# Performance work log

Hardware: AMD Instinct MI355X
Metric: run time of the kernel (lower is better)

## Reference

```python
import jax, jax.numpy as jnp
import numpy as np

D_MODEL, N_STATE, E_INNER, K_CONV, DT_RANK = 1024, 16, 2048, 4, 64
EPS = 1e-6

def _silu(x):
    return x * jax.nn.sigmoid(x)

def _rmsnorm(x, w):
    var = jnp.mean(x * x, axis=-1, keepdims=True)
    return x * jax.lax.rsqrt(var + EPS) * w

def _causal_dwconv(x, conv_w):
    # x: [B, L, E]; conv_w: [E, 1, K] depthwise kernel
    xc = jnp.swapaxes(x, 1, 2)  # [B, E, L]
    xc = jnp.pad(xc, ((0, 0), (0, 0), (K_CONV - 1, 0)))
    y = jax.lax.conv_general_dilated(
        xc, conv_w, window_strides=(1,), padding='VALID',
        dimension_numbers=('NCL', 'OIL', 'NCL'), feature_group_count=E_INNER)
    return jnp.swapaxes(y, 1, 2)  # [B, L, E]

def _selective_scan(u, delta, A, Bm, Cm, Dp):
    # u, delta: [B, L, E]; Bm, Cm: [B, L, N]; A: [E, N]; Dp: [E]
    def step(h, inp):
        d_t, B_t, C_t, u_t = inp  # [B,E], [B,N], [B,N], [B,E]
        dA = jnp.exp(d_t[..., None] * A)                       # [B,E,N]
        h = dA * h + (d_t * u_t)[..., None] * B_t[:, None, :]  # [B,E,N]
        y = jnp.einsum('ben,bn->be', h, C_t)
        return h, y
    h0 = jnp.zeros((u.shape[0], E_INNER, N_STATE), u.dtype)
    xs = (jnp.swapaxes(delta, 0, 1), jnp.swapaxes(Bm, 0, 1),
          jnp.swapaxes(Cm, 0, 1), jnp.swapaxes(u, 0, 1))
    h_last, ys = jax.lax.scan(step, h0, xs)
    return jnp.swapaxes(ys, 0, 1) + u * Dp, h_last

def setup_inputs() -> dict:
    key = jax.random.key(0)
    ks = jax.random.split(key, 8)
    B, L = 4, 1024
    hidden_states = jax.random.normal(ks[0], (B, L, D_MODEL), jnp.float32)
    norm_w = jnp.ones((D_MODEL,), jnp.float32)
    W_in = jax.random.normal(ks[1], (D_MODEL, 2 * E_INNER), jnp.float32) * (D_MODEL ** -0.5)
    conv_w = jax.random.normal(ks[2], (E_INNER, 1, K_CONV), jnp.float32) * (K_CONV ** -0.5)
    W_x = jax.random.normal(ks[3], (E_INNER, DT_RANK + 2 * N_STATE), jnp.float32) * (E_INNER ** -0.5)
    W_dt = jax.random.normal(ks[4], (DT_RANK, E_INNER), jnp.float32) * (DT_RANK ** -0.5)
    # dt bias so softplus(b) lands roughly in [delta_min, delta_max]
    dt = jnp.exp(jax.random.uniform(ks[5], (E_INNER,)) * (np.log(0.1) - np.log(0.001)) + np.log(0.001))
    b_dt = dt + jnp.log(-jnp.expm1(-dt))  # inverse softplus
    A_log = jnp.log(jnp.broadcast_to(jnp.arange(1, N_STATE + 1, dtype=jnp.float32), (E_INNER, N_STATE)))
    D_param = jnp.ones((E_INNER,), jnp.float32)
    W_out = jax.random.normal(ks[6], (E_INNER, D_MODEL), jnp.float32) * (E_INNER ** -0.5)
    return {"hidden_states": hidden_states, "norm_w": norm_w, "W_in": W_in,
            "conv_w": conv_w, "W_x": W_x, "W_dt": W_dt, "b_dt": b_dt,
            "A_log": A_log, "D_param": D_param, "W_out": W_out}

def reference(hidden_states, norm_w, W_in, conv_w, W_x, W_dt, b_dt, A_log, D_param, W_out):
    residual = hidden_states
    x = _rmsnorm(hidden_states, norm_w)
    xz = jnp.einsum('bld,de->ble', x, W_in)          # [B,L,2E]
    x_in, z = jnp.split(xz, 2, axis=-1)
    x_act = _silu(_causal_dwconv(x_in, conv_w))      # [B,L,E]
    x_db = jnp.einsum('ble,er->blr', x_act, W_x)     # [B,L,R+2N]
    dt_lr = x_db[..., :DT_RANK]
    Bm = x_db[..., DT_RANK:DT_RANK + N_STATE]
    Cm = x_db[..., DT_RANK + N_STATE:]
    delta = jax.nn.softplus(jnp.einsum('blr,re->ble', dt_lr, W_dt) + b_dt)
    A = -jnp.exp(A_log)
    y, h_last = _selective_scan(x_act, delta, A, Bm, Cm, D_param)
    y = y * _silu(z)
    out = jnp.einsum('ble,ed->bld', y, W_out)
    # dropout is identity in eval mode
    return residual + out, h_last
```

## Files before the change

### kernel.cpp

```cpp
#include <hip/hip_runtime.h>
#include <cstdint>
#include <cstddef>

#define DM 1024
#define EI 2048
#define NS 16
#define DR 64
#define BB 4
#define LL 1024
#define MM (BB*LL)
#define NCHUNK 32
#define CHUNK 32

typedef __attribute__((ext_vector_type(8))) __bf16 bf16x8;
typedef __attribute__((ext_vector_type(4))) float f32x4;
typedef __attribute__((ext_vector_type(8))) unsigned short u16x8;

__device__ __forceinline__ unsigned short f2bf(float f) {
    union { float f; unsigned int u; } v; v.f = f;
    unsigned int r = v.u + 0x7FFFu + ((v.u >> 16) & 1u);
    return (unsigned short)(r >> 16);
}
__device__ __forceinline__ float bf2f(unsigned short u) {
    union { unsigned int u; float f; } v; v.u = ((unsigned int)u) << 16;
    return v.f;
}

__device__ __forceinline__ void gload_lds16(const unsigned short* g, unsigned short* l) {
    __builtin_amdgcn_global_load_lds(
        (const __attribute__((address_space(1))) unsigned int*)g,
        (__attribute__((address_space(3))) unsigned int*)l, 16, 0, 0);
}

__global__ void rmsnorm_bf16(const float* __restrict__ x, const float* __restrict__ w,
                             unsigned short* __restrict__ out) {
    int m = blockIdx.x, tid = threadIdx.x;
    const float4* row = (const float4*)(x + (size_t)m * DM);
    float4 v = row[tid];
    float ss = v.x*v.x + v.y*v.y + v.z*v.z + v.w*v.w;
    #pragma unroll
    for (int o = 32; o; o >>= 1) ss += __shfl_down(ss, o);
    __shared__ float red[4];
    if ((tid & 63) == 0) red[tid >> 6] = ss;
    __syncthreads();
    ss = red[0] + red[1] + red[2] + red[3];
    float scale = rsqrtf(ss * (1.0f / DM) + 1e-6f);
    const float4* wr = (const float4*)w;
    float4 wv = wr[tid];
    ushort4 o4;
    o4.x = f2bf(v.x * scale * wv.x);
    o4.y = f2bf(v.y * scale * wv.y);
    o4.z = f2bf(v.z * scale * wv.z);
    o4.w = f2bf(v.w * scale * wv.w);
    ((ushort4*)out)[(size_t)m * (DM/4) + tid] = o4;
}

__global__ void transpose_all(const float* __restrict__ W_in, const float* __restrict__ W_x,
                              const float* __restrict__ W_dt, const float* __restrict__ W_out,
                              unsigned short* __restrict__ wt_in, unsigned short* __restrict__ wt_x,
                              unsigned short* __restrict__ wt_dt, unsigned short* __restrict__ wt_out) {
    __shared__ float t[32][33];
    int id = blockIdx.x;
    const float* in; unsigned short* out;
    int R, C, Cpad, bx, by;
    if (id < 4096)      { in = W_in;  out = wt_in;  R = 1024; C = 4096; Cpad = 4096; bx = id & 127; by = id >> 7; }
    else if (id < 4352) { id -= 4096; in = W_x;  out = wt_x;  R = 2048; C = 96;  Cpad = 128;  bx = id & 3;  by = id >> 2; }
    else if (id < 4480) { id -= 4352; in = W_dt; out = wt_dt; R = 64;   C = 2048; Cpad = 2048; bx = id & 63; by = id >> 6; }
    else                { id -= 4480; in = W_out; out = wt_out; R = 2048; C = 1024; Cpad = 1024; bx = id & 31; by = id >> 5; }
    int c0 = bx * 32, r0 = by * 32;
    int tx = threadIdx.x, ty = threadIdx.y;
    #pragma unroll
    for (int j = 0; j < 32; j += 8) {
        int r = r0 + ty + j, c = c0 + tx;
        t[ty + j][tx] = (r < R && c < C) ? in[(size_t)r * C + c] : 0.f;
    }
    __syncthreads();
    #pragma unroll
    for (int j = 0; j < 32; j += 8) {
        int c = c0 + ty + j, r = r0 + tx;
        if (c < Cpad && r < R) out[(size_t)c * R + r] = f2bf(t[tx][ty + j]);
    }
}

template<int EPI>
__global__ void gemm_mfma(const unsigned short* __restrict__ A,
                          const unsigned short* __restrict__ Bt,
                          float* __restrict__ C,
                          const float* __restrict__ ex1,
                          unsigned short* __restrict__ exb,
                          int M, int N, int K, int ldc) {
    __shared__ __attribute__((aligned(16))) unsigned short lds_a[128 * 32];
    __shared__ __attribute__((aligned(16))) unsigned short lds_b[128 * 32];
    const int tid = threadIdx.x;
    const int w = tid >> 6, lane = tid & 63;
    const int m0 = blockIdx.y * 128;
    const int n0 = (EPI == 3) ? 0 : blockIdx.x * 128;
    const int kstart = (EPI == 3) ? blockIdx.x * (K >> 3) : 0;
    const int kend   = (EPI == 3) ? kstart + (K >> 3) : K;
    const int wm = (w & 1) * 64, wn = (w >> 1) * 64;
    const int q = lane >> 4, r = lane & 15;
    const int srow = lane >> 2;
    const int scol = (lane & 3) * 8;

    f32x4 acc[4][4];
    f32x4 zero = {0.f, 0.f, 0.f, 0.f};
    #pragma unroll
    for (int i = 0; i < 4; ++i)
        #pragma unroll
        for (int j = 0; j < 4; ++j) acc[i][j] = zero;

    for (int kb = kstart; kb < kend; kb += 32) {
        __syncthreads();
        #pragma unroll
        for (int j = 0; j < 2; ++j) {
            int rbase = w * 32 + j * 16;
            gload_lds16(A  + (size_t)(m0 + rbase + srow) * K + kb + scol, lds_a + rbase * 32);
            gload_lds16(Bt + (size_t)(n0 + rbase + srow) * K + kb + scol, lds_b + rbase * 32);
        }
        __syncthreads();
        bf16x8 af[4], bfr[4];
        #pragma unroll
        for (int mi = 0; mi < 4; ++mi)
            af[mi] = *(const bf16x8*)(lds_a + (wm + mi * 16 + r) * 32 + q * 8);
        #pragma unroll
        for (int ni = 0; ni < 4; ++ni)
            bfr[ni] = *(const bf16x8*)(lds_b + (wn + ni * 16 + r) * 32 + q * 8);
        #pragma unroll
        for (int mi = 0; mi < 4; ++mi)
            #pragma unroll
            for (int ni = 0; ni < 4; ++ni)
                acc[mi][ni] = __builtin_amdgcn_mfma_f32_16x16x32_bf16(af[mi], bfr[ni], acc[mi][ni], 0, 0, 0);
    }

    #pragma unroll
    for (int mi = 0; mi < 4; ++mi) {
        #pragma unroll
        for (int ni = 0; ni < 4; ++ni) {
            f32x4 v = acc[mi][ni];
            int gmb = m0 + wm + mi * 16 + q * 4;
            int gn  = n0 + wn + ni * 16 + r;
            #pragma unroll
            for (int t = 0; t < 4; ++t) {
                int gm = gmb + t;
                float val = v[t];
                if (EPI == 1) {
                    C[(size_t)gm * ldc + gn] = val + ex1[(size_t)gm * ldc + gn];
                } else if (EPI == 2) {
                    val += ex1[gn];
                    val = fmaxf(val, 0.f) + log1pf(__expf(-fabsf(val)));
                    exb[(size_t)gm * ldc + gn] = f2bf(val);
                } else if (EPI == 3) {
                    C[((size_t)blockIdx.x * M + gm) * 128 + gn] = val;
                } else {
                    exb[(size_t)gm * ldc + gn] = f2bf(val);
                }
            }
        }
    }
}

__global__ void xproj_reduce(const float* __restrict__ Pp,
                             unsigned short* __restrict__ dtlr, float* __restrict__ bc) {
    int id = blockIdx.x * 256 + threadIdx.x;
    int n = id & 127, m = id >> 7;
    if (n >= DR + 2 * NS) return;
    float s = 0.f;
    #pragma unroll
    for (int ks = 0; ks < 8; ++ks)
        s += Pp[((size_t)ks * MM + m) * 128 + n];
    if (n < DR) dtlr[(size_t)m * DR + n] = f2bf(s);
    else bc[(size_t)m * 32 + (n - DR)] = s;
}

__global__ void conv_silu8(const unsigned short* __restrict__ xzb, const float* __restrict__ cw,
                           unsigned short* __restrict__ xab) {
    size_t idx8 = ((size_t)blockIdx.x * 256 + threadIdx.x) * 8;
    int e = (int)(idx8 & (EI - 1));
    size_t m = idx8 >> 11;
    int l = (int)(m & (LL - 1));
    u16x8 x0 = *(const u16x8*)(xzb + m * 4096 + e);
    u16x8 zer = {0,0,0,0,0,0,0,0};
    u16x8 x1 = (l >= 1) ? *(const u16x8*)(xzb + (m - 1) * 4096 + e) : zer;
    u16x8 x2 = (l >= 2) ? *(const u16x8*)(xzb + (m - 2) * 4096 + e) : zer;
    u16x8 x3 = (l >= 3) ? *(const u16x8*)(xzb + (m - 3) * 4096 + e) : zer;
    u16x8 o;
    #pragma unroll
    for (int j = 0; j < 8; ++j) {
        float4 wv = ((const float4*)cw)[e + j];
        float s = bf2f(x0[j]) * wv.w + bf2f(x1[j]) * wv.z
                + bf2f(x2[j]) * wv.y + bf2f(x3[j]) * wv.x;
        float a = s / (1.f + __expf(-s));
        o[j] = f2bf(a);
    }
    *(u16x8*)(xab + idx8) = o;
}

__global__ void scan_phase1(const unsigned short* __restrict__ dbufb, const unsigned short* __restrict__ xu,
                            const float* __restrict__ bc, const float* __restrict__ A_log,
                            float* __restrict__ P, float* __restrict__ H) {
    int e = blockIdx.x * 256 + threadIdx.x;
    int c = blockIdx.y, b = blockIdx.z;
    float A[NS], h[NS], p[NS];
    #pragma unroll
    for (int n = 0; n < NS; ++n) {
        A[n] = -expf(A_log[(size_t)e * NS + n]);
        h[n] = 0.f; p[n] = 1.f;
    }
    int mbase = b * LL + c * CHUNK;
    for (int t = 0; t < CHUNK; ++t) {
        size_t m = (size_t)(mbase + t);
        float d = bf2f(dbufb[m * 2048 + e]);
        float u = bf2f(xu[m * 2048 + e]);
        float du = d * u;
        const float* Bv = bc + m * 32;
        #pragma unroll
        for (int n = 0; n < NS; ++n) {
            float dA = __expf(d * A[n]);
            p[n] *= dA;
            h[n] = fmaf(dA, h[n], du * Bv[n]);
        }
    }
    size_t base = ((size_t)(b * NCHUNK + c) * NS) * 2048 + e;
    #pragma unroll
    for (int n = 0; n < NS; ++n) {
        P[base + (size_t)n * 2048] = p[n];
        H[base + (size_t)n * 2048] = h[n];
    }
}

__global__ void scan_phase2(const float* __restrict__ P, const float* __restrict__ H,
                            float* __restrict__ h0, float* __restrict__ hlast) {
    int id = blockIdx.x * 256 + threadIdx.x;
    int e = id & (EI - 1);
    int bn = id >> 11;
    int n = bn & (NS - 1), b = bn >> 4;
    float h = 0.f;
    #pragma unroll
    for (int c = 0; c < NCHUNK; ++c) {
        size_t ix = (((size_t)(b * NCHUNK + c) * NS) + n) * 2048 + e;
        h0[ix] = h;
        h = fmaf(P[ix], h, H[ix]);
    }
    hlast[(((size_t)b * EI + e) * NS) + n] = h;
}

__global__ void scan_phase3(const unsigned short* __restrict__ dbufb, const unsigned short* __restrict__ xu,
                            const unsigned short* __restrict__ xzb,
                            const float* __restrict__ bc, const float* __restrict__ A_log,
                            const float* __restrict__ Dp, const float* __restrict__ h0,
                            unsigned short* __restrict__ ybf) {
    int e = blockIdx.x * 256 + threadIdx.x;
    int c = blockIdx.y, b = blockIdx.z;
    float A[NS], h[NS];
    size_t base = ((size_t)(b * NCHUNK + c) * NS) * 2048 + e;
    #pragma unroll
    for (int n = 0; n < NS; ++n) {
        A[n] = -expf(A_log[(size_t)e * NS + n]);
        h[n] = h0[base + (size_t)n * 2048];
    }
    float D = Dp[e];
    int mbase = b * LL + c * CHUNK;
    for (int t = 0; t < CHUNK; ++t) {
        size_t m = (size_t)(mbase + t);
        float d = bf2f(dbufb[m * 2048 + e]);
        float u = bf2f(xu[m * 2048 + e]);
        float du = d * u;
        const float* Bv = bc + m * 32;
        float y = 0.f;
        #pragma unroll
        for (int n = 0; n < NS; ++n) {
            float dA = __expf(d * A[n]);
            h[n] = fmaf(dA, h[n], du * Bv[n]);
            y = fmaf(h[n], Bv[16 + n], y);
        }
        y = fmaf(u, D, y);
        float z = bf2f(xzb[m * 4096 + 2048 + e]);
        float sil = z / (1.f + __expf(-z));
        ybf[m * 2048 + e] = f2bf(y * sil);
    }
}

extern "C" void kernel_launch(void* const* d_in, const int* in_sizes, int n_in,
                              void* d_out, int out_size, void* d_ws, size_t ws_size,
                              hipStream_t stream) {
    (void)in_sizes; (void)n_in; (void)out_size; (void)ws_size;
    const float* hidden = (const float*)d_in[0];
    const float* norm_w = (const float*)d_in[1];
    const float* W_in   = (const float*)d_in[2];
    const float* conv_w = (const float*)d_in[3];
    const float* W_x    = (const float*)d_in[4];
    const float* W_dt   = (const float*)d_in[5];
    const float* b_dt   = (const float*)d_in[6];
    const float* A_log  = (const float*)d_in[7];
    const float* D_par  = (const float*)d_in[8];
    const float* W_out  = (const float*)d_in[9];
    float* out = (float*)d_out;
    char* ws = (char*)d_ws;
    const size_t MB = 1ull << 20;

    unsigned short* xzb      = (unsigned short*)(ws + 0);
    unsigned short* xact_bf  = (unsigned short*)(ws + 32 * MB);
    unsigned short* xnorm_bf = (unsigned short*)(ws + 48 * MB);
    unsigned short* wt_in    = (unsigned short*)(ws + 56 * MB);
    unsigned short* wt_out   = (unsigned short*)(ws + 64 * MB);
    unsigned short* wt_x     = (unsigned short*)(ws + 68 * MB);
    unsigned short* wt_dt    = (unsigned short*)(ws + 68 * MB + 512 * 1024);
    unsigned short* dtlr     = (unsigned short*)(ws + 69 * MB);
    float*          bc       = (float*)(ws + 69 * MB + 512 * 1024);
    unsigned short* dbufb    = (unsigned short*)(ws + 70 * MB);
    unsigned short* ybf      = (unsigned short*)(ws + 86 * MB);
    float*          h0       = (float*)(ws + 102 * MB);
    float*          P        = (float*)(ws + 118 * MB);
    float*          Hb       = (float*)(ws + 134 * MB);
    float* Ppart = P;
    float* hlast = out + (size_t)MM * DM;

    rmsnorm_bf16<<<MM, 256, 0, stream>>>(hidden, norm_w, xnorm_bf);
    transpose_all<<<6528, dim3(32, 8), 0, stream>>>(W_in, W_x, W_dt, W_out,
                                                    wt_in, wt_x, wt_dt, wt_out);

    gemm_mfma<4><<<dim3(32, 32), 256, 0, stream>>>(xnorm_bf, wt_in, nullptr, nullptr, xzb,
                                                   MM, 4096, 1024, 4096);
    conv_silu8<<<(MM * EI) / (256 * 8), 256, 0, stream>>>(xzb, conv_w, xact_bf);
    gemm_mfma<3><<<dim3(8, 32), 256, 0, stream>>>(xact_bf, wt_x, Ppart, nullptr, nullptr,
                                                  MM, 128, 2048, 128);
    xproj_reduce<<<(MM * 128) / 256, 256, 0, stream>>>(Ppart, dtlr, bc);
    gemm_mfma<2><<<dim3(16, 32), 256, 0, stream>>>(dtlr, wt_dt, nullptr, b_dt, dbufb,
                                                   MM, 2048, 64, 2048);
    scan_phase1<<<dim3(8, NCHUNK, BB), 256, 0, stream>>>(dbufb, xact_bf, bc, A_log, P, Hb);
    scan_phase2<<<(BB * NS * EI) / 256, 256, 0, stream>>>(P, Hb, h0, hlast);
    scan_phase3<<<dim3(8, NCHUNK, BB), 256, 0, stream>>>(dbufb, xact_bf, xzb, bc, A_log, D_par, h0, ybf);
    gemm_mfma<1><<<dim3(8, 32), 256, 0, stream>>>(ybf, wt_out, out, hidden, nullptr,
                                                  MM, 1024, 2048, 1024);
}
```

Baseline: 329.3 us.

## Replace in_proj GEMM with 256x256-tile 8-wave pipelined MFMA kernel

Adds a dedicated GEMM for the input projection (4096x4096x1024, bf16). It uses 256x256 tiles, 512 threads, a double-buffered LDS fed by direct global-to-LDS loads, XOR-swizzled layouts, and four phases per K step that interleave staging with MFMA bursts under raised priority. The intent is higher MFMA utilisation and more data reuse than the generic 128x128 kernel. In exchange it launches only 256 blocks with 128 KB of LDS each, which may leave some CUs idle, and it hard-codes the problem dimensions.

```diff
diff --git a/kernel.cpp b/kernel.cpp
--- a/kernel.cpp
+++ b/kernel.cpp
@@ -79,6 +79,131 @@
     for (int j = 0; j < 32; j += 8) {
         int c = c0 + ty + j, r = r0 + tx;
         if (c < Cpad && r < R) out[(size_t)c * R + r] = f2bf(t[tx][ty + j]);
+    }
+}
+
+__global__ __launch_bounds__(512, 2)
+void gemm256_8ph(const unsigned short* __restrict__ A,
+                 const unsigned short* __restrict__ Bt,
+                 unsigned short* __restrict__ C) {
+    __shared__ __attribute__((aligned(16))) unsigned short lds[65536];
+    const int tid = threadIdx.x;
+    const int w = tid >> 6, lane = tid & 63;
+    const int wm = w >> 2, wn = w & 3;
+    const int m0 = blockIdx.y * 256, n0 = blockIdx.x * 256;
+    const int r = lane & 15;
+    const int psl = ((lane >> 4) ^ ((lane >> 1) & 3)) * 8;
+    const int aoff = (wm * 128 + r) * 32 + psl;
+    const int boff = (wn * 64 + r) * 32 + psl;
+    const int c0 = w * 2;
+    const int srow = lane >> 2;
+    const int scol = ((lane & 3) ^ ((lane >> 3) & 3)) * 8;
+
+    f32x4 acc[8][4];
+    f32x4 zero = {0.f, 0.f, 0.f, 0.f};
+    #pragma unroll
+    for (int i = 0; i < 8; ++i)
+        #pragma unroll
+        for (int j = 0; j < 4; ++j) acc[i][j] = zero;
+
+    auto stage = [&](const unsigned short* __restrict__ G, int row0, int mat, int t, int ks) {
+        const unsigned short* g = G + (size_t)(row0 + c0 * 16 + srow) * 1024 + t * 64 + ks * 32 + scol;
+        unsigned short* l = lds + (t & 1) * 32768 + mat * 16384 + ks * 8192 + c0 * 512;
+        gload_lds16(g, l);
+        gload_lds16(g + 16 * 1024, l + 512);
+    };
+
+    stage(Bt, n0, 1, 0, 0); stage(A, m0, 0, 0, 0);
+    stage(Bt, n0, 1, 0, 1); stage(A, m0, 0, 0, 1);
+    stage(Bt, n0, 1, 1, 0); stage(A, m0, 0, 1, 0);
+    stage(Bt, n0, 1, 1, 1);
+    asm volatile("s_waitcnt vmcnt(6)" ::: "memory");
+    __builtin_amdgcn_s_barrier();
+    asm volatile("" ::: "memory");
+
+    for (int t = 0; t < 16; ++t) {
+        const unsigned short* la = lds + (t & 1) * 32768;
+        const unsigned short* lb = la + 16384;
+        bf16x8 af[4], bq[4];
+
+        #pragma unroll
+        for (int i = 0; i < 4; ++i) af[i] = *(const bf16x8*)(la + aoff + i * 512);
+        #pragma unroll
+        for (int j = 0; j < 4; ++j) bq[j] = *(const bf16x8*)(lb + boff + j * 512);
+        if (t + 1 < 16) stage(A, m0, 0, t + 1, 1);
+        __builtin_amdgcn_s_barrier();
+        asm volatile("" ::: "memory");
+        __builtin_amdgcn_s_setprio(1);
+        #pragma unroll
+        for (int i = 0; i < 4; ++i)
+            #pragma unroll
+            for (int j = 0; j < 4; ++j)
+                acc[i][j] = __builtin_amdgcn_mfma_f32_16x16x32_bf16(af[i], bq[j], acc[i][j], 0, 0, 0);
+        __builtin_amdgcn_s_setprio(0);
+        __builtin_amdgcn_s_barrier();
+        asm volatile("" ::: "memory");
+
+        #pragma unroll
+        for (int i = 0; i < 4; ++i) af[i] = *(const bf16x8*)(la + aoff + (4 + i) * 512);
+        if (t + 2 < 16) stage(Bt, n0, 1, t + 2, 0);
+        __builtin_amdgcn_s_barrier();
+        asm volatile("" ::: "memory");
+        __builtin_amdgcn_s_setprio(1);
+        #pragma unroll
+        for (int i = 0; i < 4; ++i)
+            #pragma unroll
+            for (int j = 0; j < 4; ++j)
+                acc[4 + i][j] = __builtin_amdgcn_mfma_f32_16x16x32_bf16(af[i], bq[j], acc[4 + i][j], 0, 0, 0);
+        __builtin_amdgcn_s_setprio(0);
+        __builtin_amdgcn_s_barrier();
+        asm volatile("" ::: "memory");
+
+        #pragma unroll
+        for (int i = 0; i < 4; ++i) af[i] = *(const bf16x8*)(la + 8192 + aoff + i * 512);
+        #pragma unroll
+        for (int j = 0; j < 4; ++j) bq[j] = *(const bf16x8*)(lb + 8192 + boff + j * 512);
+        if (t + 2 < 16) stage(A, m0, 0, t + 2, 0);
+        __builtin_amdgcn_s_barrier();
+        asm volatile("" ::: "memory");
+        __builtin_amdgcn_s_setprio(1);
+        #pragma unroll
+        for (int i = 0; i < 4; ++i)
+            #pragma unroll
+            for (int j = 0; j < 4; ++j)
+                acc[i][j] = __builtin_amdgcn_mfma_f32_16x16x32_bf16(af[i], bq[j], acc[i][j], 0, 0, 0);
+        __builtin_amdgcn_s_setprio(0);
+        __builtin_amdgcn_s_barrier();
+        asm volatile("" ::: "memory");
+
+        #pragma unroll
+        for (int i = 0; i < 4; ++i) af[i] = *(const bf16x8*)(la + 8192 + aoff + (4 + i) * 512);
+        if (t + 2 < 16) stage(Bt, n0, 1, t + 2, 1);
+        __builtin_amdgcn_s_barrier();
+        asm volatile("" ::: "memory");
+        __builtin_amdgcn_s_setprio(1);
+        #pragma unroll
+        for (int i = 0; i < 4; ++i)
+            #pragma unroll
+            for (int j = 0; j < 4; ++j)
+                acc[4 + i][j] = __builtin_amdgcn_mfma_f32_16x16x32_bf16(af[i], bq[j], acc[4 + i][j], 0, 0, 0);
+        __builtin_amdgcn_s_setprio(0);
+        if (t + 2 < 16) { asm volatile("s_waitcnt vmcnt(6)" ::: "memory"); }
+        else            { asm volatile("s_waitcnt vmcnt(0)" ::: "memory"); }
+        __builtin_amdgcn_s_barrier();
+        asm volatile("" ::: "memory");
+    }
+
+    const int q4 = (lane >> 4) * 4;
+    #pragma unroll
+    for (int mi = 0; mi < 8; ++mi) {
+        #pragma unroll
+        for (int nj = 0; nj < 4; ++nj) {
+            int gm = m0 + wm * 128 + mi * 16 + q4;
+            int gn = n0 + wn * 64 + nj * 16 + r;
+            #pragma unroll
+            for (int tt = 0; tt < 4; ++tt)
+                C[(size_t)(gm + tt) * 4096 + gn] = f2bf(acc[mi][nj][tt]);
+        }
     }
 }
 
@@ -319,8 +444,7 @@
     transpose_all<<<6528, dim3(32, 8), 0, stream>>>(W_in, W_x, W_dt, W_out,
                                                     wt_in, wt_x, wt_dt, wt_out);
 
-    gemm_mfma<4><<<dim3(32, 32), 256, 0, stream>>>(xnorm_bf, wt_in, nullptr, nullptr, xzb,
-                                                   MM, 4096, 1024, 4096);
+    gemm256_8ph<<<dim3(16, 16), 512, 0, stream>>>(xnorm_bf, wt_in, xzb);
     conv_silu8<<<(MM * EI) / (256 * 8), 256, 0, stream>>>(xzb, conv_w, xact_bf);
     gemm_mfma<3><<<dim3(8, 32), 256, 0, stream>>>(xact_bf, wt_x, Ppart, nullptr, nullptr,
                                                   MM, 128, 2048, 128);
```

Result: no change. 325.5 us (-1.2%).
